# Kernel tuning notes

Hardware: AMD Instinct MI355X
Metric: run time of the kernel (lower is better)

## Reference

```python
import jax, jax.numpy as jnp
import numpy as np
from jax.scipy.special import gammaln

N_I = 100000
N_J = 100000
D = 8
S_I = 6000
S_J = 6000
NNZ = 500000
EPS = 1e-06


def setup_inputs() -> dict:
    key = jax.random.key(0)
    ks = jax.random.split(key, 9)
    beta = jax.random.normal(ks[0], (N_I,), dtype=jnp.float32)
    gamma = jax.random.normal(ks[1], (N_J,), dtype=jnp.float32)
    latent_zi = jax.random.normal(ks[2], (N_I, D), dtype=jnp.float32)
    latent_zj = jax.random.normal(ks[3], (N_J, D), dtype=jnp.float32)
    # multinomial-without-replacement node samples -> random permutation prefix
    sample_i_idx = jax.random.permutation(ks[4], N_I)[:S_I]
    sample_j_idx = jax.random.permutation(ks[5], N_J)[:S_J]
    # spspmm-selected subgraph links (global node indices) with edge counts
    sparse_i_sample = jax.random.randint(ks[6], (NNZ,), 0, N_I)
    sparse_j_sample = jax.random.randint(ks[7], (NNZ,), 0, N_J)
    valueC = jax.random.uniform(ks[8], (NNZ,), dtype=jnp.float32)
    return {
        'beta': beta, 'gamma': gamma,
        'latent_zi': latent_zi, 'latent_zj': latent_zj,
        'valueC': valueC,
        'sample_i_idx': sample_i_idx, 'sample_j_idx': sample_j_idx,
        'sparse_i_sample': sparse_i_sample, 'sparse_j_sample': sparse_j_sample,
    }


def reference(beta, gamma, latent_zi, latent_zj, valueC,
              sample_i_idx, sample_j_idx, sparse_i_sample, sparse_j_sample):
    # Dense non-link term over sampled (I, J) block
    zi = latent_zi[sample_i_idx]            # [S_I, D]
    zj = latent_zj[sample_j_idx]            # [S_J, D]
    diff = zi[:, None, :] - zj[None, :, :] + EPS   # [S_I, S_J, D]
    z_dist = jnp.sqrt(jnp.sum(diff * diff, axis=-1))  # [S_I, S_J]
    Lambda = beta[sample_i_idx][:, None] + gamma[sample_j_idx][None, :] - z_dist
    # Sparse link terms (Poisson log-likelihood)
    dl = latent_zi[sparse_i_sample] - latent_zj[sparse_j_sample] + EPS  # [NNZ, D]
    z_dist_links = jnp.sqrt(jnp.sum(dl * dl, axis=-1))                  # [NNZ]
    bias_links = beta[sparse_i_sample] + gamma[sparse_j_sample]
    log_Lambda_links = valueC * (bias_links - z_dist_links)
    LL = jnp.sum(log_Lambda_links - gammaln(valueC + 1.0)) - jnp.sum(jnp.exp(Lambda))
    return LL
```

## Files before the change

### kernel.cpp

```cpp
#include <hip/hip_runtime.h>
#include <hip/hip_fp16.h>
#include <math.h>

#define NI_TOT 100000
#define NJ_TOT 100000
#define DD 8
#define SI_N 6000
#define SJ_N 6000
#define NNZ_N 500000
#define EPSF 1e-6f
#define LOG2E 1.44269504088896f
#define INV_LOG2E 0.693147180559945f

#define TI 64
#define JPT 4
#define JTILE (256 * JPT)
#define ND_I ((SI_N + TI - 1) / TI)
#define NJT ((SJ_N + JTILE - 1) / JTILE)
#define N_DENSE_BLOCKS (ND_I * NJT)
#define LPT 4
#define SPARSE_SPAN (256 * LPT)
#define N_SPARSE_BLOCKS ((NNZ_N + SPARSE_SPAN - 1) / SPARSE_SPAN)
#define N_TOTAL_BLOCKS (N_DENSE_BLOCKS + N_SPARSE_BLOCKS)

#define NROWS (NI_TOT + NJ_TOT)
#define HZ_BYTES ((size_t)NROWS * DD * 2)
#define HB_BYTES ((size_t)NROWS * 2)
#define WS_NEED (HZ_BYTES + HB_BYTES)

#define GA1 (-0.577191652f)
#define GA2 ( 0.988205891f)
#define GA3 (-0.897056937f)
#define GA4 ( 0.918206857f)
#define GA5 (-0.756704078f)
#define GA6 ( 0.482199394f)
#define GA7 (-0.193527818f)
#define GA8 ( 0.035868343f)

__global__ __launch_bounds__(256) void pack_kernel(
    const float* __restrict__ beta, const float* __restrict__ gamma,
    const float* __restrict__ zi_all, const float* __restrict__ zj_all,
    __half* __restrict__ hz, __half* __restrict__ hb, float* __restrict__ out)
{
    const int r = blockIdx.x * 256 + threadIdx.x;
    if (r == 0) out[0] = 0.0f;
    if (r < NROWS) {
        const float* src = (r < NI_TOT) ? zi_all + (size_t)r * DD
                                        : zj_all + (size_t)(r - NI_TOT) * DD;
        float4 a = ((const float4*)src)[0];
        float4 b = ((const float4*)src)[1];
        __half2 h0 = __floats2half2_rn(a.x, a.y);
        __half2 h1 = __floats2half2_rn(a.z, a.w);
        __half2 h2 = __floats2half2_rn(b.x, b.y);
        __half2 h3 = __floats2half2_rn(b.z, b.w);
        uint4 u;
        u.x = *(unsigned*)&h0; u.y = *(unsigned*)&h1;
        u.z = *(unsigned*)&h2; u.w = *(unsigned*)&h3;
        ((uint4*)hz)[r] = u;
    } else if (r < 2 * NROWS) {
        const int q = r - NROWS;
        float v = (q < NI_TOT) ? beta[q] : gamma[q - NI_TOT];
        hb[q] = __float2half(v);
    }
}

__device__ __forceinline__ void unpack_row(uint4 u, float f[DD]) {
    float2 p;
    p = __half22float2(*(__half2*)&u.x); f[0] = p.x; f[1] = p.y;
    p = __half22float2(*(__half2*)&u.y); f[2] = p.x; f[3] = p.y;
    p = __half22float2(*(__half2*)&u.z); f[4] = p.x; f[5] = p.y;
    p = __half22float2(*(__half2*)&u.w); f[6] = p.x; f[7] = p.y;
}

__global__ __launch_bounds__(256) void fused_kernel(
    const float* __restrict__ beta, const float* __restrict__ gamma,
    const float* __restrict__ zi_all, const float* __restrict__ zj_all,
    const float* __restrict__ valueC,
    const int* __restrict__ si, const int* __restrict__ sj,
    const int* __restrict__ spi, const int* __restrict__ spj,
    const __half* __restrict__ hz, const __half* __restrict__ hb,
    float* __restrict__ out, int mode)
{
    __shared__ float sRed[4];
    __shared__ __align__(16) float  sZi[TI * DD];
    __shared__ __align__(8)  float2 sIB[TI];

    const int t = threadIdx.x;
    float blocksum = 0.0f;

    if (blockIdx.x >= N_SPARSE_BLOCKS) {
        const int db = blockIdx.x - N_SPARSE_BLOCKS;
        const int it = db % ND_I;
        const int js = db / ND_I;
        const int i0 = it * TI;

        for (int idx = t; idx < TI * DD; idx += 256) {
            int r = idx >> 3, d = idx & 7;
            int gi = i0 + r;
            float v = (gi < SI_N) ? zi_all[(size_t)si[gi] * DD + d] : 0.0f;
            sZi[idx] = (v + EPSF) * (-2.0f * LOG2E);
        }
        __syncthreads();
        if (t < TI) {
            int gi = i0 + t;
            float s = 0.0f;
#pragma unroll
            for (int d = 0; d < DD; ++d) {
                float m = sZi[t * DD + d];
                s = fmaf(m, m, s);
            }
            float eb = 0.0f;
            if (gi < SI_N) eb = __builtin_amdgcn_exp2f(beta[si[gi]] * LOG2E);
            sIB[t] = make_float2(0.25f * s, eb);
        }

        const int jb = js * JTILE + t * JPT;
        float zc[JPT][DD], s2[JPT], gf[JPT];
#pragma unroll
        for (int u = 0; u < JPT; ++u) {
            int gj = jb + u;
            if (gj < SJ_N) {
                int row = sj[gj];
                const float4* q = (const float4*)(zj_all + (size_t)row * DD);
                float4 q0 = q[0], q1 = q[1];
                zc[u][0]=q0.x*LOG2E; zc[u][1]=q0.y*LOG2E; zc[u][2]=q0.z*LOG2E; zc[u][3]=q0.w*LOG2E;
                zc[u][4]=q1.x*LOG2E; zc[u][5]=q1.y*LOG2E; zc[u][6]=q1.z*LOG2E; zc[u][7]=q1.w*LOG2E;
                gf[u] = __builtin_amdgcn_exp2f(gamma[row] * LOG2E);
            } else {
#pragma unroll
                for (int d = 0; d < DD; ++d) zc[u][d] = 0.0f;
                gf[u] = 0.0f;
            }
            float s = 0.0f;
#pragma unroll
            for (int d = 0; d < DD; ++d) s = fmaf(zc[u][d], zc[u][d], s);
            s2[u] = s;
        }
        __syncthreads();

        float acc[JPT] = {0.0f, 0.0f, 0.0f, 0.0f};
        float4 cr0 = *(const float4*)&sZi[0];
        float4 cr1 = *(const float4*)&sZi[4];
        float2 cib = sIB[0];
#pragma unroll 4
        for (int a = 0; a < TI; ++a) {
            float4 nr0, nr1; float2 nib;
            if (a + 1 < TI) {
                nr0 = *(const float4*)&sZi[(a + 1) * DD];
                nr1 = *(const float4*)&sZi[(a + 1) * DD + 4];
                nib = sIB[a + 1];
            }
#pragma unroll
            for (int u = 0; u < JPT; ++u) {
                float dd;
                dd = fmaf(cr0.x, zc[u][0], cib.x);
                dd = fmaf(cr0.y, zc[u][1], dd);
                dd = fmaf(cr0.z, zc[u][2], dd);
                dd = fmaf(cr0.w, zc[u][3], dd);
                dd = fmaf(cr1.x, zc[u][4], dd);
                dd = fmaf(cr1.y, zc[u][5], dd);
                dd = fmaf(cr1.z, zc[u][6], dd);
                dd = fmaf(cr1.w, zc[u][7], dd);
                float ss = fmaxf(dd + s2[u], 1e-20f);
                float dist = __builtin_amdgcn_sqrtf(ss);
                float e = __builtin_amdgcn_exp2f(-dist);
                acc[u] = fmaf(cib.y, e, acc[u]);
            }
            cr0 = nr0; cr1 = nr1; cib = nib;
        }
        float bs = 0.0f;
#pragma unroll
        for (int u = 0; u < JPT; ++u) bs = fmaf(gf[u], acc[u], bs);
        blocksum = -bs;
    } else {
        const int base = blockIdx.x * SPARSE_SPAN + t;
        float val = 0.0f;
        const uint4* hzv = (const uint4*)hz;
#pragma unroll
        for (int u = 0; u < LPT; ++u) {
            const int idx = base + u * 256;
            if (idx >= NNZ_N) continue;
            const int i = spi[idx], j = spj[idx];
            const float c = valueC[idx];
            float dist, bg;
            if (mode == 0) {
                uint4 ui = hzv[i];
                uint4 uj = hzv[NI_TOT + j];
                float fi[DD], fj[DD];
                unpack_row(ui, fi);
                unpack_row(uj, fj);
                float ss = 0.0f;
#pragma unroll
                for (int d = 0; d < DD; ++d) {
                    float df = fi[d] - fj[d] + EPSF;
                    ss = fmaf(df, df, ss);
                }
                ss = fmaxf(ss, 1e-20f);
                dist = __builtin_amdgcn_sqrtf(ss);
                bg = __half2float(hb[i]) + __half2float(hb[NI_TOT + j]);
            } else {
                const float4* zi4 = (const float4*)(zi_all + (size_t)i * DD);
                const float4* zj4 = (const float4*)(zj_all + (size_t)j * DD);
                float4 a0 = zi4[0], a1 = zi4[1];
                float4 b0 = zj4[0], b1 = zj4[1];
                float ss = 0.0f, df;
                df = a0.x-b0.x+EPSF; ss = fmaf(df,df,ss);
                df = a0.y-b0.y+EPSF; ss = fmaf(df,df,ss);
                df = a0.z-b0.z+EPSF; ss = fmaf(df,df,ss);
                df = a0.w-b0.w+EPSF; ss = fmaf(df,df,ss);
                df = a1.x-b1.x+EPSF; ss = fmaf(df,df,ss);
                df = a1.y-b1.y+EPSF; ss = fmaf(df,df,ss);
                df = a1.z-b1.z+EPSF; ss = fmaf(df,df,ss);
                df = a1.w-b1.w+EPSF; ss = fmaf(df,df,ss);
                ss = fmaxf(ss, 1e-20f);
                dist = __builtin_amdgcn_sqrtf(ss);
                bg = beta[i] + gamma[j];
            }
            float g = 1.0f + c*(GA1 + c*(GA2 + c*(GA3 + c*(GA4 + c*(GA5
                          + c*(GA6 + c*(GA7 + c*GA8)))))));
            val += c * (bg - dist) - __builtin_amdgcn_logf(g) * INV_LOG2E;
        }
        blocksum = val;
    }

    float acc = blocksum;
#pragma unroll
    for (int off = 32; off; off >>= 1) acc += __shfl_down(acc, off, 64);
    const int lane = t & 63, w = t >> 6;
    if (lane == 0) sRed[w] = acc;
    __syncthreads();
    if (t == 0) {
        float s = sRed[0] + sRed[1] + sRed[2] + sRed[3];
        atomicAdd(out, s);
    }
}

extern "C" void kernel_launch(void* const* d_in, const int* in_sizes, int n_in,
                              void* d_out, int out_size, void* d_ws, size_t ws_size,
                              hipStream_t stream) {
    const float* beta   = (const float*)d_in[0];
    const float* gamma  = (const float*)d_in[1];
    const float* zi     = (const float*)d_in[2];
    const float* zj     = (const float*)d_in[3];
    const float* valueC = (const float*)d_in[4];
    const int* si   = (const int*)d_in[5];
    const int* sjx  = (const int*)d_in[6];
    const int* spi  = (const int*)d_in[7];
    const int* spj  = (const int*)d_in[8];
    float* out = (float*)d_out;

    if (d_ws && ws_size >= WS_NEED) {
        __half* hz = (__half*)d_ws;
        __half* hb = (__half*)((char*)d_ws + HZ_BYTES);
        const int packb = (2 * NROWS + 255) / 256;
        pack_kernel<<<packb, 256, 0, stream>>>(beta, gamma, zi, zj, hz, hb, out);
        fused_kernel<<<N_TOTAL_BLOCKS, 256, 0, stream>>>(
            beta, gamma, zi, zj, valueC, si, sjx, spi, spj, hz, hb, out, 0);
    } else {
        hipMemsetAsync(out, 0, sizeof(float), stream);
        fused_kernel<<<N_TOTAL_BLOCKS, 256, 0, stream>>>(
            beta, gamma, zi, zj, valueC, si, sjx, spi, spj,
            (const __half*)zi, (const __half*)zi, out, 1);
    }
}
```

Before: 118.1 us.

## Halve per-thread work, schedule dense blocks first, replace atomics with partial reduction

Cuts columns per thread in the dense tile and links per thread in the sparse path from 4 to 2, doubling block counts to raise occupancy and balance across CUs. Dense blocks are now indexed first so the heavy work is dispatched early. The single global atomicAdd per block is replaced by per-block partials in workspace plus a one-block final reduction kernel, making the sum deterministic and removing atomic contention. The cost is an extra kernel launch and more blocks that each reload the shared i-tile.

```diff
diff --git a/kernel.cpp b/kernel.cpp
--- a/kernel.cpp
+++ b/kernel.cpp
@@ -13,12 +13,12 @@
 #define INV_LOG2E 0.693147180559945f
 
 #define TI 64
-#define JPT 4
+#define JPT 2
 #define JTILE (256 * JPT)
 #define ND_I ((SI_N + TI - 1) / TI)
 #define NJT ((SJ_N + JTILE - 1) / JTILE)
 #define N_DENSE_BLOCKS (ND_I * NJT)
-#define LPT 4
+#define LPT 2
 #define SPARSE_SPAN (256 * LPT)
 #define N_SPARSE_BLOCKS ((NNZ_N + SPARSE_SPAN - 1) / SPARSE_SPAN)
 #define N_TOTAL_BLOCKS (N_DENSE_BLOCKS + N_SPARSE_BLOCKS)
@@ -26,7 +26,7 @@
 #define NROWS (NI_TOT + NJ_TOT)
 #define HZ_BYTES ((size_t)NROWS * DD * 2)
 #define HB_BYTES ((size_t)NROWS * 2)
-#define WS_NEED (HZ_BYTES + HB_BYTES)
+#define PARTIALS_OFF (HZ_BYTES + HB_BYTES)
 
 #define GA1 (-0.577191652f)
 #define GA2 ( 0.988205891f)
@@ -40,10 +40,9 @@
 __global__ __launch_bounds__(256) void pack_kernel(
     const float* __restrict__ beta, const float* __restrict__ gamma,
     const float* __restrict__ zi_all, const float* __restrict__ zj_all,
-    __half* __restrict__ hz, __half* __restrict__ hb, float* __restrict__ out)
+    __half* __restrict__ hz, __half* __restrict__ hb)
 {
     const int r = blockIdx.x * 256 + threadIdx.x;
-    if (r == 0) out[0] = 0.0f;
     if (r < NROWS) {
         const float* src = (r < NI_TOT) ? zi_all + (size_t)r * DD
                                         : zj_all + (size_t)(r - NI_TOT) * DD;
@@ -79,7 +78,7 @@
     const int* __restrict__ si, const int* __restrict__ sj,
     const int* __restrict__ spi, const int* __restrict__ spj,
     const __half* __restrict__ hz, const __half* __restrict__ hb,
-    float* __restrict__ out, int mode)
+    float* __restrict__ partials, float* __restrict__ out, int mode)
 {
     __shared__ float sRed[4];
     __shared__ __align__(16) float  sZi[TI * DD];
@@ -88,10 +87,9 @@
     const int t = threadIdx.x;
     float blocksum = 0.0f;
 
-    if (blockIdx.x >= N_SPARSE_BLOCKS) {
-        const int db = blockIdx.x - N_SPARSE_BLOCKS;
-        const int it = db % ND_I;
-        const int js = db / ND_I;
+    if (blockIdx.x < N_DENSE_BLOCKS) {
+        const int it = blockIdx.x % ND_I;
+        const int js = blockIdx.x / ND_I;
         const int i0 = it * TI;
 
         for (int idx = t; idx < TI * DD; idx += 256) {
@@ -138,7 +136,7 @@
         }
         __syncthreads();
 
-        float acc[JPT] = {0.0f, 0.0f, 0.0f, 0.0f};
+        float acc[JPT] = {0.0f, 0.0f};
         float4 cr0 = *(const float4*)&sZi[0];
         float4 cr1 = *(const float4*)&sZi[4];
         float2 cib = sIB[0];
@@ -173,7 +171,7 @@
         for (int u = 0; u < JPT; ++u) bs = fmaf(gf[u], acc[u], bs);
         blocksum = -bs;
     } else {
-        const int base = blockIdx.x * SPARSE_SPAN + t;
+        const int base = (blockIdx.x - N_DENSE_BLOCKS) * SPARSE_SPAN + t;
         float val = 0.0f;
         const uint4* hzv = (const uint4*)hz;
 #pragma unroll
@@ -231,8 +229,28 @@
     __syncthreads();
     if (t == 0) {
         float s = sRed[0] + sRed[1] + sRed[2] + sRed[3];
-        atomicAdd(out, s);
-    }
+        if (mode) atomicAdd(out, s);
+        else partials[blockIdx.x] = s;
+    }
+}
+
+__global__ __launch_bounds__(256) void final_reduce_kernel(
+    const float* __restrict__ p, int n, float* __restrict__ out)
+{
+    __shared__ float sRed[4];
+    float s0 = 0.0f, s1 = 0.0f, s2 = 0.0f, s3 = 0.0f;
+    int i = threadIdx.x;
+    for (; i + 768 < n; i += 1024) {
+        s0 += p[i]; s1 += p[i + 256]; s2 += p[i + 512]; s3 += p[i + 768];
+    }
+    for (; i < n; i += 256) s0 += p[i];
+    float s = (s0 + s1) + (s2 + s3);
+#pragma unroll
+    for (int off = 32; off; off >>= 1) s += __shfl_down(s, off, 64);
+    const int lane = threadIdx.x & 63, w = threadIdx.x >> 6;
+    if (lane == 0) sRed[w] = s;
+    __syncthreads();
+    if (threadIdx.x == 0) out[0] = sRed[0] + sRed[1] + sRed[2] + sRed[3];
 }
 
 extern "C" void kernel_launch(void* const* d_in, const int* in_sizes, int n_in,
@@ -249,17 +267,22 @@
     const int* spj  = (const int*)d_in[8];
     float* out = (float*)d_out;
 
-    if (d_ws && ws_size >= WS_NEED) {
+    const int ntot = N_TOTAL_BLOCKS;
+    const size_t need = PARTIALS_OFF + (size_t)ntot * sizeof(float);
+
+    if (d_ws && ws_size >= need) {
         __half* hz = (__half*)d_ws;
         __half* hb = (__half*)((char*)d_ws + HZ_BYTES);
+        float* p = (float*)((char*)d_ws + PARTIALS_OFF);
         const int packb = (2 * NROWS + 255) / 256;
-        pack_kernel<<<packb, 256, 0, stream>>>(beta, gamma, zi, zj, hz, hb, out);
-        fused_kernel<<<N_TOTAL_BLOCKS, 256, 0, stream>>>(
-            beta, gamma, zi, zj, valueC, si, sjx, spi, spj, hz, hb, out, 0);
+        pack_kernel<<<packb, 256, 0, stream>>>(beta, gamma, zi, zj, hz, hb);
+        fused_kernel<<<ntot, 256, 0, stream>>>(
+            beta, gamma, zi, zj, valueC, si, sjx, spi, spj, hz, hb, p, out, 0);
+        final_reduce_kernel<<<1, 256, 0, stream>>>(p, ntot, out);
     } else {
         hipMemsetAsync(out, 0, sizeof(float), stream);
-        fused_kernel<<<N_TOTAL_BLOCKS, 256, 0, stream>>>(
+        fused_kernel<<<ntot, 256, 0, stream>>>(
             beta, gamma, zi, zj, valueC, si, sjx, spi, spj,
-            (const __half*)zi, (const __half*)zi, out, 1);
-    }
-}
+            (const __half*)zi, (const __half*)zi, nullptr, out, 1);
+    }
+}
```

Measured after the change: 106.0 us. 10.3% less time.

## Precompute i-row records in pack kernel, drop LDS staging, use ticket reduction

Applied to the files above, without the earlier changes.

The pack kernel now also precomputes the scaled i-side latent rows, their squared-norm seeds and exp(beta) into a global record array. The dense blocks read these records directly from global memory inside the inner loop instead of staging them in LDS behind two barriers. Per-thread work per block is halved (JPT and LPT go from 4 to 2), so more blocks run. The float atomicAdd is replaced by per-block partials plus a last-block ticket reduction, which gives a deterministic sum. The cost is a larger pack kernel and inner-loop global loads that depend on cache hits.

```diff
diff --git a/kernel.cpp b/kernel.cpp
--- a/kernel.cpp
+++ b/kernel.cpp
@@ -13,12 +13,12 @@
 #define INV_LOG2E 0.693147180559945f
 
 #define TI 64
-#define JPT 4
+#define JPT 2
 #define JTILE (256 * JPT)
 #define ND_I ((SI_N + TI - 1) / TI)
 #define NJT ((SJ_N + JTILE - 1) / JTILE)
 #define N_DENSE_BLOCKS (ND_I * NJT)
-#define LPT 4
+#define LPT 2
 #define SPARSE_SPAN (256 * LPT)
 #define N_SPARSE_BLOCKS ((NNZ_N + SPARSE_SPAN - 1) / SPARSE_SPAN)
 #define N_TOTAL_BLOCKS (N_DENSE_BLOCKS + N_SPARSE_BLOCKS)
@@ -26,7 +26,12 @@
 #define NROWS (NI_TOT + NJ_TOT)
 #define HZ_BYTES ((size_t)NROWS * DD * 2)
 #define HB_BYTES ((size_t)NROWS * 2)
-#define WS_NEED (HZ_BYTES + HB_BYTES)
+#define IREC_N (ND_I * TI)
+#define IREC_OFF (HZ_BYTES + HB_BYTES)
+#define IREC_BYTES ((size_t)IREC_N * 12 * 4)
+#define PART_OFF (IREC_OFF + IREC_BYTES)
+#define TICKET_OFF (PART_OFF + (size_t)N_TOTAL_BLOCKS * 4)
+#define WS_NEED (TICKET_OFF + 4)
 
 #define GA1 (-0.577191652f)
 #define GA2 ( 0.988205891f)
@@ -40,10 +45,12 @@
 __global__ __launch_bounds__(256) void pack_kernel(
     const float* __restrict__ beta, const float* __restrict__ gamma,
     const float* __restrict__ zi_all, const float* __restrict__ zj_all,
-    __half* __restrict__ hz, __half* __restrict__ hb, float* __restrict__ out)
+    const int* __restrict__ si,
+    __half* __restrict__ hz, __half* __restrict__ hb,
+    float* __restrict__ irec, unsigned* __restrict__ ticket)
 {
     const int r = blockIdx.x * 256 + threadIdx.x;
-    if (r == 0) out[0] = 0.0f;
+    if (r == 0) *ticket = 0u;
     if (r < NROWS) {
         const float* src = (r < NI_TOT) ? zi_all + (size_t)r * DD
                                         : zj_all + (size_t)(r - NI_TOT) * DD;
@@ -61,6 +68,31 @@
         const int q = r - NROWS;
         float v = (q < NI_TOT) ? beta[q] : gamma[q - NI_TOT];
         hb[q] = __float2half(v);
+    } else if (r < 2 * NROWS + IREC_N) {
+        const int q = r - 2 * NROWS;
+        float4 m0 = make_float4(0.f, 0.f, 0.f, 0.f);
+        float4 m1 = make_float4(0.f, 0.f, 0.f, 0.f);
+        float seed = 0.f, eb = 0.f;
+        if (q < SI_N) {
+            const int row = si[q];
+            const float4* zp = (const float4*)(zi_all + (size_t)row * DD);
+            float4 a = zp[0], b = zp[1];
+            const float k = -2.0f * LOG2E;
+            m0.x = (a.x + EPSF) * k; m0.y = (a.y + EPSF) * k;
+            m0.z = (a.z + EPSF) * k; m0.w = (a.w + EPSF) * k;
+            m1.x = (b.x + EPSF) * k; m1.y = (b.y + EPSF) * k;
+            m1.z = (b.z + EPSF) * k; m1.w = (b.w + EPSF) * k;
+            float s = 0.f;
+            s = fmaf(m0.x, m0.x, s); s = fmaf(m0.y, m0.y, s);
+            s = fmaf(m0.z, m0.z, s); s = fmaf(m0.w, m0.w, s);
+            s = fmaf(m1.x, m1.x, s); s = fmaf(m1.y, m1.y, s);
+            s = fmaf(m1.z, m1.z, s); s = fmaf(m1.w, m1.w, s);
+            seed = 0.25f * s;
+            eb = __builtin_amdgcn_exp2f(beta[row] * LOG2E);
+        }
+        float4* op = (float4*)(irec + (size_t)q * 12);
+        op[0] = m0; op[1] = m1;
+        op[2] = make_float4(seed, eb, 0.f, 0.f);
     }
 }
 
@@ -72,6 +104,45 @@
     p = __half22float2(*(__half2*)&u.w); f[6] = p.x; f[7] = p.y;
 }
 
+template<int MODE>
+__device__ __forceinline__ void load_irow(
+    const float* __restrict__ irp, int a,
+    const float* __restrict__ zi_all, const float* __restrict__ beta,
+    const int* __restrict__ si, int i0,
+    float4& r0, float4& r1, float4& r2)
+{
+    if (MODE == 0) {
+        const float* p = irp + (size_t)a * 12;
+        r0 = *(const float4*)p;
+        r1 = *(const float4*)(p + 4);
+        r2 = *(const float4*)(p + 8);
+    } else {
+        const int gi = i0 + a;
+        if (gi < SI_N) {
+            const int row = si[gi];
+            const float4* zp = (const float4*)(zi_all + (size_t)row * DD);
+            float4 za = zp[0], zb = zp[1];
+            const float k = -2.0f * LOG2E;
+            r0.x = (za.x + EPSF) * k; r0.y = (za.y + EPSF) * k;
+            r0.z = (za.z + EPSF) * k; r0.w = (za.w + EPSF) * k;
+            r1.x = (zb.x + EPSF) * k; r1.y = (zb.y + EPSF) * k;
+            r1.z = (zb.z + EPSF) * k; r1.w = (zb.w + EPSF) * k;
+            float s = 0.f;
+            s = fmaf(r0.x, r0.x, s); s = fmaf(r0.y, r0.y, s);
+            s = fmaf(r0.z, r0.z, s); s = fmaf(r0.w, r0.w, s);
+            s = fmaf(r1.x, r1.x, s); s = fmaf(r1.y, r1.y, s);
+            s = fmaf(r1.z, r1.z, s); s = fmaf(r1.w, r1.w, s);
+            r2 = make_float4(0.25f * s,
+                             __builtin_amdgcn_exp2f(beta[row] * LOG2E), 0.f, 0.f);
+        } else {
+            r0 = make_float4(0.f, 0.f, 0.f, 0.f);
+            r1 = r0;
+            r2 = r0;
+        }
+    }
+}
+
+template<int MODE>
 __global__ __launch_bounds__(256) void fused_kernel(
     const float* __restrict__ beta, const float* __restrict__ gamma,
     const float* __restrict__ zi_all, const float* __restrict__ zj_all,
@@ -79,40 +150,21 @@
     const int* __restrict__ si, const int* __restrict__ sj,
     const int* __restrict__ spi, const int* __restrict__ spj,
     const __half* __restrict__ hz, const __half* __restrict__ hb,
-    float* __restrict__ out, int mode)
+    const float* __restrict__ irec,
+    float* __restrict__ partials, unsigned* __restrict__ ticket,
+    float* __restrict__ out)
 {
     __shared__ float sRed[4];
-    __shared__ __align__(16) float  sZi[TI * DD];
-    __shared__ __align__(8)  float2 sIB[TI];
+    __shared__ int lastFlag;
 
     const int t = threadIdx.x;
     float blocksum = 0.0f;
 
-    if (blockIdx.x >= N_SPARSE_BLOCKS) {
-        const int db = blockIdx.x - N_SPARSE_BLOCKS;
-        const int it = db % ND_I;
-        const int js = db / ND_I;
+    if (blockIdx.x < N_DENSE_BLOCKS) {
+        const int it = blockIdx.x % ND_I;
+        const int js = blockIdx.x / ND_I;
         const int i0 = it * TI;
-
-        for (int idx = t; idx < TI * DD; idx += 256) {
-            int r = idx >> 3, d = idx & 7;
-            int gi = i0 + r;
-            float v = (gi < SI_N) ? zi_all[(size_t)si[gi] * DD + d] : 0.0f;
-            sZi[idx] = (v + EPSF) * (-2.0f * LOG2E);
-        }
-        __syncthreads();
-        if (t < TI) {
-            int gi = i0 + t;
-            float s = 0.0f;
-#pragma unroll
-            for (int d = 0; d < DD; ++d) {
-                float m = sZi[t * DD + d];
-                s = fmaf(m, m, s);
-            }
-            float eb = 0.0f;
-            if (gi < SI_N) eb = __builtin_amdgcn_exp2f(beta[si[gi]] * LOG2E);
-            sIB[t] = make_float2(0.25f * s, eb);
-        }
+        const float* irp = irec + (size_t)i0 * 12;
 
         const int jb = js * JTILE + t * JPT;
         float zc[JPT][DD], s2[JPT], gf[JPT];
@@ -136,24 +188,19 @@
             for (int d = 0; d < DD; ++d) s = fmaf(zc[u][d], zc[u][d], s);
             s2[u] = s;
         }
-        __syncthreads();
-
-        float acc[JPT] = {0.0f, 0.0f, 0.0f, 0.0f};
-        float4 cr0 = *(const float4*)&sZi[0];
-        float4 cr1 = *(const float4*)&sZi[4];
-        float2 cib = sIB[0];
+
+        float acc[JPT] = {0.0f, 0.0f};
+        float4 cr0, cr1, cr2;
+        load_irow<MODE>(irp, 0, zi_all, beta, si, i0, cr0, cr1, cr2);
 #pragma unroll 4
         for (int a = 0; a < TI; ++a) {
-            float4 nr0, nr1; float2 nib;
-            if (a + 1 < TI) {
-                nr0 = *(const float4*)&sZi[(a + 1) * DD];
-                nr1 = *(const float4*)&sZi[(a + 1) * DD + 4];
-                nib = sIB[a + 1];
-            }
+            float4 nr0, nr1, nr2;
+            if (a + 1 < TI)
+                load_irow<MODE>(irp, a + 1, zi_all, beta, si, i0, nr0, nr1, nr2);
 #pragma unroll
             for (int u = 0; u < JPT; ++u) {
                 float dd;
-                dd = fmaf(cr0.x, zc[u][0], cib.x);
+                dd = fmaf(cr0.x, zc[u][0], cr2.x);
                 dd = fmaf(cr0.y, zc[u][1], dd);
                 dd = fmaf(cr0.z, zc[u][2], dd);
                 dd = fmaf(cr0.w, zc[u][3], dd);
@@ -164,16 +211,16 @@
                 float ss = fmaxf(dd + s2[u], 1e-20f);
                 float dist = __builtin_amdgcn_sqrtf(ss);
                 float e = __builtin_amdgcn_exp2f(-dist);
-                acc[u] = fmaf(cib.y, e, acc[u]);
+                acc[u] = fmaf(cr2.y, e, acc[u]);
             }
-            cr0 = nr0; cr1 = nr1; cib = nib;
+            cr0 = nr0; cr1 = nr1; cr2 = nr2;
         }
         float bs = 0.0f;
 #pragma unroll
         for (int u = 0; u < JPT; ++u) bs = fmaf(gf[u], acc[u], bs);
         blocksum = -bs;
     } else {
-        const int base = blockIdx.x * SPARSE_SPAN + t;
+        const int base = (blockIdx.x - N_DENSE_BLOCKS) * SPARSE_SPAN + t;
         float val = 0.0f;
         const uint4* hzv = (const uint4*)hz;
 #pragma unroll
@@ -183,7 +230,7 @@
             const int i = spi[idx], j = spj[idx];
             const float c = valueC[idx];
             float dist, bg;
-            if (mode == 0) {
+            if (MODE == 0) {
                 uint4 ui = hzv[i];
                 uint4 uj = hzv[NI_TOT + j];
                 float fi[DD], fj[DD];
@@ -229,9 +276,31 @@
     const int lane = t & 63, w = t >> 6;
     if (lane == 0) sRed[w] = acc;
     __syncthreads();
-    if (t == 0) {
-        float s = sRed[0] + sRed[1] + sRed[2] + sRed[3];
-        atomicAdd(out, s);
+
+    if (MODE == 0) {
+        if (t == 0) {
+            float s = sRed[0] + sRed[1] + sRed[2] + sRed[3];
+            partials[blockIdx.x] = s;
+            __threadfence();
+            unsigned tk = atomicAdd(ticket, 1u);
+            lastFlag = (tk == (unsigned)(N_TOTAL_BLOCKS - 1));
+        }
+        __syncthreads();
+        if (lastFlag) {
+            __threadfence();
+            float s = 0.0f;
+            for (int i2 = t; i2 < N_TOTAL_BLOCKS; i2 += 256) s += partials[i2];
+#pragma unroll
+            for (int off = 32; off; off >>= 1) s += __shfl_down(s, off, 64);
+            if (lane == 0) sRed[w] = s;
+            __syncthreads();
+            if (t == 0) out[0] = sRed[0] + sRed[1] + sRed[2] + sRed[3];
+        }
+    } else {
+        if (t == 0) {
+            float s = sRed[0] + sRed[1] + sRed[2] + sRed[3];
+            atomicAdd(out, s);
+        }
     }
 }
 
@@ -252,14 +321,19 @@
     if (d_ws && ws_size >= WS_NEED) {
         __half* hz = (__half*)d_ws;
         __half* hb = (__half*)((char*)d_ws + HZ_BYTES);
-        const int packb = (2 * NROWS + 255) / 256;
-        pack_kernel<<<packb, 256, 0, stream>>>(beta, gamma, zi, zj, hz, hb, out);
-        fused_kernel<<<N_TOTAL_BLOCKS, 256, 0, stream>>>(
-            beta, gamma, zi, zj, valueC, si, sjx, spi, spj, hz, hb, out, 0);
+        float* irec = (float*)((char*)d_ws + IREC_OFF);
+        float* p = (float*)((char*)d_ws + PART_OFF);
+        unsigned* ticket = (unsigned*)((char*)d_ws + TICKET_OFF);
+        const int packb = (2 * NROWS + IREC_N + 255) / 256;
+        pack_kernel<<<packb, 256, 0, stream>>>(beta, gamma, zi, zj, si,
+                                               hz, hb, irec, ticket);
+        fused_kernel<0><<<N_TOTAL_BLOCKS, 256, 0, stream>>>(
+            beta, gamma, zi, zj, valueC, si, sjx, spi, spj,
+            hz, hb, irec, p, ticket, out);
     } else {
         hipMemsetAsync(out, 0, sizeof(float), stream);
-        fused_kernel<<<N_TOTAL_BLOCKS, 256, 0, stream>>>(
+        fused_kernel<1><<<N_TOTAL_BLOCKS, 256, 0, stream>>>(
             beta, gamma, zi, zj, valueC, si, sjx, spi, spj,
-            (const __half*)zi, (const __half*)zi, out, 1);
-    }
-}
+            nullptr, nullptr, nullptr, nullptr, nullptr, out);
+    }
+}
```

Result: slower. 148.2 us (+25.4%).
